# Performance work log

Hardware: AMD Instinct MI355X
Metric: run time of the kernel (lower is better)

The kernel has to match this reference:

```python
import jax, jax.numpy as jnp
import numpy as np
from jax import lax

KERNEL_SIZE = 2  # init kwarg erode_kernel


def _min_filter_same(x, k):
    """Separable k x k min-filter (erosion) over the last two dims of NCHW x,
    SAME output size, out-of-bounds padded with +inf (matches cv2.erode's
    default border value, which never wins the min)."""
    inf = jnp.asarray(jnp.inf, x.dtype)
    # rows pass then cols pass; square min-filter is separable
    y = lax.reduce_window(x, inf, lax.min,
                          window_dimensions=(1, 1, k, 1),
                          window_strides=(1, 1, 1, 1),
                          padding='SAME')
    y = lax.reduce_window(y, inf, lax.min,
                          window_dimensions=(1, 1, 1, k),
                          window_strides=(1, 1, 1, 1),
                          padding='SAME')
    return y


def setup_inputs() -> dict:
    key = jax.random.key(0)
    x = jax.random.normal(key, (32, 3, 512, 512), dtype=jnp.float32)
    return {"x": x, "l": 1, "gpu": 0}


def reference(x, l, gpu):
    # iterations_times = 4 * (l + 2 - 1); erosion window grows by 2*iters
    iterations_times = 4 * (l + 1)
    k = KERNEL_SIZE + 2 * iterations_times  # 18 for l=1
    # original: tensor2pil(e * 0.5 + 0.5) -> cv2.erode -> pil2tensor ([0,1])
    # (uint8 quantization of the PIL round-trip is omitted; same min-filter math)
    y = x * 0.5 + 0.5
    y = _min_filter_same(y, k)
    return y
```

## Files before the change

### kernel.cpp

```cpp
#include <hip/hip_runtime.h>


#define IMG 512

__device__ __forceinline__ float4 f4min(float4 a, float4 b) {
    return make_float4(fminf(a.x, b.x), fminf(a.y, b.y),
                       fminf(a.z, b.z), fminf(a.w, b.w));
}

__global__ __launch_bounds__(256, 3)
void erode_fused_22187801051678(const float* __restrict__ in,
                                float* __restrict__ out) {
    __shared__ float4 B4[64][38];

    const int tid = threadIdx.x;
    const int w0 = blockIdx.x * 128;
    const int h0 = blockIdx.y * 64;
    const size_t plane = (size_t)blockIdx.z * (size_t)(IMG * IMG);

    const float4 VINF = make_float4(__builtin_inff(), __builtin_inff(),
                                    __builtin_inff(), __builtin_inff());

    for (int u = tid; u < 296; u += 256) {
        const int c = u % 37;
        const int s = u / 37;
        const int cb = w0 - 8 + 4 * c;
        const bool wok = (unsigned)cb < (unsigned)IMG;
        const int cbc = min(max(cb, 0), IMG - 4);
        const int rbase = h0 + 8 * s - 8;
        const float* bp = in + plane + cbc;

        float4 X[25];
#pragma unroll
        for (int i = 0; i < 25; ++i) {
            const int ghc = min(max(rbase + i, 0), IMG - 1);
            X[i] = *reinterpret_cast<const float4*>(bp + (size_t)ghc * IMG);
        }
        __builtin_amdgcn_sched_barrier(0);

#pragma unroll
        for (int i = 0; i < 25; ++i) {
            const int gh = rbase + i;
            if (!(wok && (unsigned)gh < (unsigned)IMG)) X[i] = VINF;
        }

        float4 S[8];
        float4 rs = X[17];
#pragma unroll
        for (int i = 16; i >= 0; --i) {
            rs = f4min(rs, X[i]);
            if (i < 8) S[i] = rs;
        }
        const int rb = 8 * s;
        B4[rb + 0][c] = S[0];
        float4 rp = X[18];
        B4[rb + 1][c] = f4min(S[1], rp);
#pragma unroll
        for (int i = 19; i <= 24; ++i) {
            rp = f4min(rp, X[i]);
            B4[rb + (i - 17)][c] = f4min(S[i - 17], rp);
        }
    }
    __syncthreads();

    const int gq = tid & 31;
    const int r0 = tid >> 5;
#pragma unroll
    for (int sw = 0; sw < 8; ++sw) {
        const int r = r0 + 8 * sw;
        float z[24];
#pragma unroll
        for (int k = 0; k < 6; ++k) {
            const float4 v = B4[r][gq + k];
            z[4 * k + 0] = v.x; z[4 * k + 1] = v.y;
            z[4 * k + 2] = v.z; z[4 * k + 3] = v.w;
        }
        const float a0 = fminf(z[3], z[4]);
        const float a1 = fminf(z[5], z[6]);
        const float a2 = fminf(z[7], z[8]);
        const float a3 = fminf(z[9], z[10]);
        const float a4 = fminf(z[11], z[12]);
        const float a5 = fminf(z[13], z[14]);
        const float a6 = fminf(z[15], z[16]);
        const float b0 = fminf(a0, a1), b1 = fminf(a2, a3);
        const float b2 = fminf(a4, a5), b3 = fminf(a6, z[17]);
        const float core = fminf(fminf(b0, b1), fminf(b2, b3));
        const float o0 = fminf(fminf(z[0], z[1]), fminf(z[2], core));
        const float o1 = fminf(fminf(z[1], z[2]), fminf(core, z[18]));
        const float o2 = fminf(fminf(z[2], core), fminf(z[18], z[19]));
        const float o3 = fminf(fminf(core, z[18]), fminf(z[19], z[20]));
        const float4 res = make_float4(o0 * 0.5f + 0.5f, o1 * 0.5f + 0.5f,
                                       o2 * 0.5f + 0.5f, o3 * 0.5f + 0.5f);
        *reinterpret_cast<float4*>(
            out + plane + (size_t)(h0 + r) * IMG + (w0 + 4 * gq)) = res;
    }
}

extern "C" void kernel_launch(void* const* d_in, const int* in_sizes, int n_in,
                              void* d_out, int out_size, void* d_ws, size_t ws_size,
                              hipStream_t stream) {
    const float* x = (const float*)d_in[0];
    float* out = (float*)d_out;
    const int planes = in_sizes[0] / (IMG * IMG);
    dim3 grid(IMG / 128, IMG / 64, planes);
    erode_fused_22187801051678<<<grid, dim3(256), 0, stream>>>(x, out);
}
```

Baseline: 188.5 us.

## Halve row tile, stream vertical min accumulation, use nontemporal stores

Cuts the block tile height from 64 to 32 rows and raises the launch-bound occupancy target from 3 to 8 blocks. The vertical pass stops holding 25 loaded rows in registers and instead folds each load straight into 8 running-min accumulators, which lowers register pressure. Output writes become nontemporal stores so they do not pollute the cache. The trade-off is more vertical halo re-reading per output row, only 148 of 256 threads active in the load phase, and a vertical pass that does more min operations than the shared prefix/suffix scheme it replaces.

```diff
diff --git a/kernel.cpp b/kernel.cpp
--- a/kernel.cpp
+++ b/kernel.cpp
@@ -2,71 +2,61 @@
 
 
 #define IMG 512
+
+typedef float f32x4 __attribute__((ext_vector_type(4)));
 
 __device__ __forceinline__ float4 f4min(float4 a, float4 b) {
     return make_float4(fminf(a.x, b.x), fminf(a.y, b.y),
                        fminf(a.z, b.z), fminf(a.w, b.w));
 }
 
-__global__ __launch_bounds__(256, 3)
+__global__ __launch_bounds__(256, 8)
 void erode_fused_22187801051678(const float* __restrict__ in,
                                 float* __restrict__ out) {
-    __shared__ float4 B4[64][38];
+    __shared__ float4 B4[32][38];
 
     const int tid = threadIdx.x;
     const int w0 = blockIdx.x * 128;
-    const int h0 = blockIdx.y * 64;
+    const int h0 = blockIdx.y * 32;
     const size_t plane = (size_t)blockIdx.z * (size_t)(IMG * IMG);
 
     const float4 VINF = make_float4(__builtin_inff(), __builtin_inff(),
                                     __builtin_inff(), __builtin_inff());
 
-    for (int u = tid; u < 296; u += 256) {
-        const int c = u % 37;
-        const int s = u / 37;
+    if (tid < 148) {
+        const int c = tid % 37;
+        const int s = tid / 37;
         const int cb = w0 - 8 + 4 * c;
         const bool wok = (unsigned)cb < (unsigned)IMG;
         const int cbc = min(max(cb, 0), IMG - 4);
         const int rbase = h0 + 8 * s - 8;
         const float* bp = in + plane + cbc;
 
-        float4 X[25];
+        float4 acc[8];
 #pragma unroll
-        for (int i = 0; i < 25; ++i) {
-            const int ghc = min(max(rbase + i, 0), IMG - 1);
-            X[i] = *reinterpret_cast<const float4*>(bp + (size_t)ghc * IMG);
-        }
-        __builtin_amdgcn_sched_barrier(0);
+        for (int j = 0; j < 8; ++j) acc[j] = VINF;
 
 #pragma unroll
         for (int i = 0; i < 25; ++i) {
             const int gh = rbase + i;
-            if (!(wok && (unsigned)gh < (unsigned)IMG)) X[i] = VINF;
-        }
-
-        float4 S[8];
-        float4 rs = X[17];
+            const int ghc = min(max(gh, 0), IMG - 1);
+            float4 x = *reinterpret_cast<const float4*>(bp + (size_t)ghc * IMG);
+            if (!(wok && (unsigned)gh < (unsigned)IMG)) x = VINF;
 #pragma unroll
-        for (int i = 16; i >= 0; --i) {
-            rs = f4min(rs, X[i]);
-            if (i < 8) S[i] = rs;
+            for (int j = 0; j < 8; ++j)
+                if (j <= i && i <= j + 17)
+                    acc[j] = f4min(acc[j], x);
         }
         const int rb = 8 * s;
-        B4[rb + 0][c] = S[0];
-        float4 rp = X[18];
-        B4[rb + 1][c] = f4min(S[1], rp);
 #pragma unroll
-        for (int i = 19; i <= 24; ++i) {
-            rp = f4min(rp, X[i]);
-            B4[rb + (i - 17)][c] = f4min(S[i - 17], rp);
-        }
+        for (int j = 0; j < 8; ++j) B4[rb + j][c] = acc[j];
     }
     __syncthreads();
 
     const int gq = tid & 31;
     const int r0 = tid >> 5;
 #pragma unroll
-    for (int sw = 0; sw < 8; ++sw) {
+    for (int sw = 0; sw < 4; ++sw) {
         const int r = r0 + 8 * sw;
         float z[24];
 #pragma unroll
@@ -89,10 +79,11 @@
         const float o1 = fminf(fminf(z[1], z[2]), fminf(core, z[18]));
         const float o2 = fminf(fminf(z[2], core), fminf(z[18], z[19]));
         const float o3 = fminf(fminf(core, z[18]), fminf(z[19], z[20]));
-        const float4 res = make_float4(o0 * 0.5f + 0.5f, o1 * 0.5f + 0.5f,
-                                       o2 * 0.5f + 0.5f, o3 * 0.5f + 0.5f);
-        *reinterpret_cast<float4*>(
-            out + plane + (size_t)(h0 + r) * IMG + (w0 + 4 * gq)) = res;
+        f32x4 res = {o0 * 0.5f + 0.5f, o1 * 0.5f + 0.5f,
+                     o2 * 0.5f + 0.5f, o3 * 0.5f + 0.5f};
+        __builtin_nontemporal_store(
+            res, reinterpret_cast<f32x4*>(
+                     out + plane + (size_t)(h0 + r) * IMG + (w0 + 4 * gq)));
     }
 }
 
@@ -102,6 +93,6 @@
     const float* x = (const float*)d_in[0];
     float* out = (float*)d_out;
     const int planes = in_sizes[0] / (IMG * IMG);
-    dim3 grid(IMG / 128, IMG / 64, planes);
+    dim3 grid(IMG / 128, IMG / 32, planes);
     erode_fused_22187801051678<<<grid, dim3(256), 0, stream>>>(x, out);
 }
```

Measured after the change: 201.0 us. 6.7% more time.
